# Kernel tuning notes

Hardware: AMD Instinct MI355X
Metric: run time of the kernel (lower is better)

Reference implementation:

```python
import jax, jax.numpy as jnp
import numpy as np

B, L, D, K, H = 2, 384, 1024, 128, 32
NUM_EDGES = 25600
NUM_T = 1000
SCALING = K ** -0.5
SQRT_2PI = float(np.sqrt(2.0 * np.pi))


def setup_inputs() -> dict:
    key = jax.random.key(0)
    ks = jax.random.split(key, 20)
    s = 0.02
    inp = {}
    inp["token_id"] = jax.random.randint(ks[0], (B, L), 0, 160)
    inp["is_periodic"] = jnp.zeros((B,), dtype=bool)
    inp["pos"] = 5.0 * jax.random.normal(ks[1], (B, L, 3), dtype=jnp.float32)
    inp["adj"] = jnp.ones((B, L, L), dtype=bool)
    inp["node_type_edge"] = jax.random.randint(ks[2], (B, L, L, 2), 0, NUM_EDGES)
    inp["time_step"] = jax.random.uniform(ks[3], (B, L), dtype=jnp.float32)
    inp["clean_mask"] = jnp.zeros((B, L), dtype=bool)
    # parameters
    inp["embed_w"] = s * jax.random.normal(ks[4], (160, D), dtype=jnp.float32)
    inp["Wpos"] = s * jax.random.normal(ks[5], (K, 3), dtype=jnp.float32)
    inp["Wpfe"] = s * jax.random.normal(ks[6], (D, K), dtype=jnp.float32)
    inp["gbf_means"] = jax.random.normal(ks[7], (K,), dtype=jnp.float32)
    inp["gbf_stds"] = 0.5 + jax.random.uniform(ks[8], (K,), dtype=jnp.float32)
    inp["gbf_mul"] = 1.0 + s * jax.random.normal(ks[9], (NUM_EDGES, 1), dtype=jnp.float32)
    inp["gbf_bias"] = s * jax.random.normal(ks[10], (NUM_EDGES, 1), dtype=jnp.float32)
    inp["W1"] = s * jax.random.normal(ks[11], (K, K), dtype=jnp.float32)
    inp["b1"] = jnp.zeros((K,), dtype=jnp.float32)
    inp["W2"] = s * jax.random.normal(ks[12], (H, K), dtype=jnp.float32)
    inp["b2"] = jnp.zeros((H,), dtype=jnp.float32)
    inp["Wproj"] = s * jax.random.normal(ks[13], (D, K), dtype=jnp.float32)
    inp["bproj"] = jnp.zeros((D,), dtype=jnp.float32)
    inp["Wt1"] = s * jax.random.normal(ks[14], (D, D), dtype=jnp.float32)
    inp["bt1"] = jnp.zeros((D,), dtype=jnp.float32)
    inp["Wt2"] = s * jax.random.normal(ks[15], (D, D), dtype=jnp.float32)
    inp["bt2"] = jnp.zeros((D,), dtype=jnp.float32)
    return inp


def _forward(token_id, is_periodic, pos, adj, node_type_edge, time_step, clean_mask,
             embed_w, Wpos, Wpfe, gbf_means, gbf_stds, gbf_mul, gbf_bias,
             W1, b1, W2, b2, Wproj, bproj, Wt1, bt1, Wt2, bt2):
    padding_mask = token_id == 0                                  # (B,L)
    molecule_mask = (token_id <= 129) & (~is_periodic[:, None])   # (B,L)
    x = embed_w[token_id]                                         # (B,L,D)

    # ---- _pos_emb (non-PBC branch: expand_pos = pos, expand_mask = padding_mask) ----
    delta = pos[:, :, None, :] - pos[:, None, :, :]               # (B,L,L,3)
    dist = jnp.sqrt(jnp.maximum(jnp.sum(delta * delta, -1), 1e-12))  # (B,L,L), safe norm

    # GaussianLayer
    mul = gbf_mul[node_type_edge].sum(-2)                         # (B,L,L,1)
    bias = gbf_bias[node_type_edge].sum(-2)                       # (B,L,L,1)
    y = mul * dist[..., None] + bias                              # (B,L,L,1) -> broadcast K
    std = jnp.abs(gbf_stds) + 1e-5
    a = (y - gbf_means) / std
    edge_feature = jnp.exp(-0.5 * a * a) / (SQRT_2PI * std)       # (B,L,L,K)

    # NonLinear projection to per-head bias
    gab = jax.nn.gelu(edge_feature @ W1.T + b1, approximate=False) @ W2.T + b2  # (B,L,L,H)
    gab = jnp.where(padding_mask[:, None, :, None], -jnp.inf, gab)  # expand-col mask
    gab = jnp.where(padding_mask[:, :, None, None], 0.0, gab)       # padding-row mask
    pos_attn_bias = jnp.transpose(gab, (0, 3, 1, 2))              # (B,H,L,L)

    d = gab.sum(-1)                                               # (B,L,L) sum over heads
    minv = jnp.finfo(jnp.float32).min
    d = jnp.where(padding_mask[:, None, :], minv, d)
    d = jnp.where(padding_mask[:, :, None], minv, d)
    adj_eff = adj | (~molecule_mask[:, :, None])
    d = jnp.where(~adj_eff, minv, d)
    attn = jax.nn.softmax(d * SCALING, axis=-1)                   # (B,L,L)

    pos_e = pos @ Wpos.T                                          # (B,L,K)
    pos_e = jnp.where(padding_mask[..., None], 0.0, pos_e)
    pfe = jnp.einsum('bij,bjk->bik', attn, pos_e)                 # (B,L,K)
    pfe = pfe @ Wpfe.T                                            # (B,L,D)

    ef = jnp.where(padding_mask[:, None, :, None], 0.0, edge_feature).sum(-2)  # (B,L,K)
    pfe = pfe + ef @ Wproj.T + bproj
    pos_embedding = jnp.where(padding_mask[..., None], 0.0, pfe)  # (B,L,D)

    # ---- time step encoder (sinusoidal + MLP) ----
    t = jnp.where(clean_mask, 0.0, time_step) * NUM_T             # (B,L)
    half = D // 2
    freqs = jnp.exp(-jnp.log(10000.0) * jnp.arange(half, dtype=jnp.float32) / half)
    ang = t[..., None] * freqs                                    # (B,L,half)
    sin_emb = jnp.concatenate([jnp.sin(ang), jnp.cos(ang)], -1)   # (B,L,D)
    time_embed = jax.nn.silu(sin_emb @ Wt1.T + bt1) @ Wt2.T + bt2

    x = x + time_embed + pos_embedding
    return x, padding_mask, time_embed, pos_attn_bias, pos_embedding


def reference(token_id, is_periodic, pos, adj, node_type_edge, time_step, clean_mask,
              embed_w, Wpos, Wpfe, gbf_means, gbf_stds, gbf_mul, gbf_bias,
              W1, b1, W2, b2, Wproj, bproj, Wt1, bt1, Wt2, bt2):
    return _forward(token_id, is_periodic, pos, adj, node_type_edge, time_step, clean_mask,
                    embed_w, Wpos, Wpfe, gbf_means, gbf_stds, gbf_mul, gbf_bias,
                    W1, b1, W2, b2, Wproj, bproj, Wt1, bt1, Wt2, bt2)
```

## Files before the change

kernel.cpp:

```cpp
#include <hip/hip_runtime.h>
#include <stddef.h>

#define B_ 2
#define L_ 384
#define D_ 1024
#define K_ 128
#define H_ 32

#define MINV (-3.402823466e38f)
#define NEG_BIG (-1.0e38f)
#define SCALING_ 0.08838834764831845f
#define INV_SQRT_2PI 0.3989422804014327f

typedef __attribute__((ext_vector_type(8))) short bf16x8;
typedef __attribute__((ext_vector_type(4))) float f32x4;

__device__ __forceinline__ float finitize(float x) {
    return fminf(fmaxf(x, -1.0e38f), 1.0e38f);
}
__device__ __forceinline__ unsigned short f2bf(float x) {
    unsigned int u = __float_as_uint(x);
    u += 0x7FFFu + ((u >> 16) & 1u);
    return (unsigned short)(u >> 16);
}
__device__ __forceinline__ unsigned short f2bf_rtz(float x) {
    return (unsigned short)(__float_as_uint(x) >> 16);
}
__device__ __forceinline__ float gelu_tanh(float x) {
    const float x2 = x * x;
    const float z = x * fmaf(0.0356774081f, x2, 0.7978845608f);
    const float e = __expf(2.0f * z);
    const float t = fmaf(-2.0f, __builtin_amdgcn_rcpf(e + 1.0f), 1.0f);
    const float hx = 0.5f * x;
    return fmaf(hx, t, hx);
}

__global__ __launch_bounds__(256) void prep_kernel(
    const float* __restrict__ W1, const float* __restrict__ W2,
    const float* __restrict__ Wpfe, const float* __restrict__ Wproj,
    const float* __restrict__ Wt1, const float* __restrict__ Wt2,
    unsigned short* __restrict__ W1bf, unsigned short* __restrict__ W2bf,
    unsigned short* __restrict__ Wpfebf, unsigned short* __restrict__ Wprojbf,
    unsigned short* __restrict__ Wt1bf, unsigned short* __restrict__ Wt2bf)
{
    const int i = blockIdx.x * 256 + threadIdx.x;
    const float* src; unsigned short* dst; int off;
    if (i < 4096)        { src = W1;    dst = W1bf;    off = i; }
    else if (i < 5120)   { src = W2;    dst = W2bf;    off = i - 4096; }
    else if (i < 37888)  { src = Wpfe;  dst = Wpfebf;  off = i - 5120; }
    else if (i < 70656)  { src = Wproj; dst = Wprojbf; off = i - 37888; }
    else if (i < 332800) { src = Wt1;   dst = Wt1bf;   off = i - 70656; }
    else if (i < 594944) { src = Wt2;   dst = Wt2bf;   off = i - 332800; }
    else return;
    const float4 v = ((const float4*)src)[off];
    ushort4 p; p.x = f2bf(v.x); p.y = f2bf(v.y); p.z = f2bf(v.z); p.w = f2bf(v.w);
    ((ushort4*)dst)[off] = p;
}

__global__ __launch_bounds__(256) void sin_kernel(const float* __restrict__ time_step,
                                                  const unsigned char* __restrict__ clean,
                                                  const int* __restrict__ token,
                                                  unsigned short* __restrict__ sin_bf,
                                                  float* __restrict__ padout)
{
    const int row = blockIdx.x;
    if (threadIdx.x == 0) padout[row] = (token[row] == 0) ? 1.0f : 0.0f;
    const float t = (clean[row] ? 0.0f : time_step[row]) * 1000.0f;
    for (int k = threadIdx.x; k < 512; k += 256) {
        const float f = __expf(-9.210340371976184f * (float)k * (1.0f / 512.0f));
        const float ang = t * f;
        sin_bf[(size_t)row * D_ + k]       = f2bf(__sinf(ang));
        sin_bf[(size_t)row * D_ + 512 + k] = f2bf(__cosf(ang));
    }
}

__global__ __launch_bounds__(256) void gemm_ts(const unsigned short* __restrict__ A,
                                               const unsigned short* __restrict__ Bw,
                                               const float* __restrict__ bias,
                                               void* __restrict__ Cv,
                                               int M, int N, int Kd, int act)
{
    __shared__ unsigned short sA[32][72];
    __shared__ unsigned short sB[64][72];
    const int tid  = threadIdx.x;
    const int lane = tid & 63;
    const int wave = tid >> 6;
    const int l15  = lane & 15;
    const int quad = lane >> 4;
    const int mt   = wave & 1;
    const int np   = wave >> 1;
    const int m0 = blockIdx.y * 32, n0 = blockIdx.x * 64;

    const int ar = tid >> 3,        ac = (tid & 7) * 8;
    const int br0 = tid >> 3,       bc0 = ac;
    const int br1 = (tid + 256) >> 3, bc1 = ac;

    f32x4 acc[2];
#pragma unroll
    for (int t = 0; t < 2; ++t) acc[t] = (f32x4){0.f, 0.f, 0.f, 0.f};

    uint4 ra  = *(const uint4*)&A[(size_t)(m0 + ar) * Kd + ac];
    uint4 rb0 = *(const uint4*)&Bw[(size_t)(n0 + br0) * Kd + bc0];
    uint4 rb1 = *(const uint4*)&Bw[(size_t)(n0 + br1) * Kd + bc1];

    for (int k0 = 0; k0 < Kd; k0 += 64) {
        *(uint4*)&sA[ar][ac]   = ra;
        *(uint4*)&sB[br0][bc0] = rb0;
        *(uint4*)&sB[br1][bc1] = rb1;
        __syncthreads();
        if (k0 + 64 < Kd) {
            ra  = *(const uint4*)&A[(size_t)(m0 + ar) * Kd + k0 + 64 + ac];
            rb0 = *(const uint4*)&Bw[(size_t)(n0 + br0) * Kd + k0 + 64 + bc0];
            rb1 = *(const uint4*)&Bw[(size_t)(n0 + br1) * Kd + k0 + 64 + bc1];
        }
#pragma unroll
        for (int kk = 0; kk < 64; kk += 32) {
            const bf16x8 av = *(const bf16x8*)&sA[mt * 16 + l15][kk + quad * 8];
#pragma unroll
            for (int t = 0; t < 2; ++t) {
                const bf16x8 bv = *(const bf16x8*)&sB[(np * 2 + t) * 16 + l15][kk + quad * 8];
                acc[t] = __builtin_amdgcn_mfma_f32_16x16x32_bf16(av, bv, acc[t], 0, 0, 0);
            }
        }
        __syncthreads();
    }
#pragma unroll
    for (int t = 0; t < 2; ++t) {
        const int nc = n0 + (np * 2 + t) * 16 + l15;
        const float bv = bias[nc];
#pragma unroll
        for (int r = 0; r < 4; ++r) {
            const int mr = m0 + mt * 16 + quad * 4 + r;
            float v = acc[t][r] + bv;
            if (act) {
                v = v / (1.0f + __expf(-v));
                ((unsigned short*)Cv)[(size_t)mr * N + nc] = f2bf(v);
            } else {
                ((float*)Cv)[(size_t)mr * N + nc] = v;
            }
        }
    }
}

__global__ __launch_bounds__(256) void pe_gemm(const unsigned short* __restrict__ pfe_bf,
                                               const unsigned short* __restrict__ ef_bf,
                                               const unsigned short* __restrict__ Wpfebf,
                                               const unsigned short* __restrict__ Wprojbf,
                                               const float* __restrict__ bproj,
                                               const int* __restrict__ token,
                                               const float* __restrict__ embed_w,
                                               const float* __restrict__ te,
                                               float* __restrict__ outPE,
                                               float* __restrict__ outX)
{
    __shared__ unsigned short sA[32][136];
    __shared__ unsigned short sB[64][136];
    const int tid  = threadIdx.x;
    const int lane = tid & 63;
    const int wave = tid >> 6;
    const int l15  = lane & 15;
    const int quad = lane >> 4;
    const int mt   = wave & 1;
    const int np   = wave >> 1;
    const int m0 = blockIdx.y * 32, n0 = blockIdx.x * 64;

    f32x4 acc[2];
#pragma unroll
    for (int t = 0; t < 2; ++t) acc[t] = (f32x4){0.f, 0.f, 0.f, 0.f};

    for (int phase = 0; phase < 2; ++phase) {
        const unsigned short* Ap = phase ? ef_bf : pfe_bf;
        const unsigned short* Bp = phase ? Wprojbf : Wpfebf;
#pragma unroll
        for (int e = tid; e < 512; e += 256) {
            const int r = e >> 4, c8 = (e & 15) * 8;
            *(uint4*)&sA[r][c8] = *(const uint4*)&Ap[(size_t)(m0 + r) * K_ + c8];
        }
#pragma unroll
        for (int e = tid; e < 1024; e += 256) {
            const int r = e >> 4, c8 = (e & 15) * 8;
            *(uint4*)&sB[r][c8] = *(const uint4*)&Bp[(size_t)(n0 + r) * K_ + c8];
        }
        __syncthreads();
#pragma unroll
        for (int ks = 0; ks < 4; ++ks) {
            const bf16x8 av = *(const bf16x8*)&sA[mt * 16 + l15][ks * 32 + quad * 8];
#pragma unroll
            for (int t = 0; t < 2; ++t) {
                const bf16x8 bv = *(const bf16x8*)&sB[(np * 2 + t) * 16 + l15][ks * 32 + quad * 8];
                acc[t] = __builtin_amdgcn_mfma_f32_16x16x32_bf16(av, bv, acc[t], 0, 0, 0);
            }
        }
        __syncthreads();
    }
#pragma unroll
    for (int t = 0; t < 2; ++t) {
        const int nc = n0 + (np * 2 + t) * 16 + l15;
        const float bv = bproj[nc];
#pragma unroll
        for (int r = 0; r < 4; ++r) {
            const int mr = m0 + mt * 16 + quad * 4 + r;
            const int tok = token[mr];
            const float pe = (tok == 0) ? 0.0f : (acc[t][r] + bv);
            outPE[(size_t)mr * D_ + nc] = pe;
            outX[(size_t)mr * D_ + nc] = embed_w[(size_t)tok * D_ + nc]
                                       + te[(size_t)mr * D_ + nc] + pe;
        }
    }
}

__global__ __launch_bounds__(256, 3) void edge_kernel(
    const int* __restrict__ token_id,
    const unsigned char* __restrict__ is_periodic,
    const float* __restrict__ pos,
    const unsigned char* __restrict__ adj,
    const int* __restrict__ nte,
    const float* __restrict__ gbf_means,
    const float* __restrict__ gbf_stds,
    const float* __restrict__ gbf_mul,
    const float* __restrict__ gbf_bias,
    const float* __restrict__ b1,
    const float* __restrict__ b2,
    const float* __restrict__ Wpos,
    const unsigned short* __restrict__ W1bf,
    const unsigned short* __restrict__ W2bf,
    unsigned short* __restrict__ pfe_bf,
    unsigned short* __restrict__ ef_bf,
    float* __restrict__ out_pab)
{
    const int bx = blockIdx.x;
    const int b = bx / L_;
    const int i = bx - b * L_;
    const int row = bx;
    const int tid = threadIdx.x;

    const int tok_i = token_id[row];
    if (tok_i == 0) {
        for (int idx = tid; idx < H_ * L_; idx += 256) {
            const int h = idx / L_;
            const int j = idx - h * L_;
            out_pab[((size_t)(b * H_ + h) * L_ + i) * L_ + j] = 0.0f;
        }
        if (tid < K_) {
            pfe_bf[(size_t)row * K_ + tid] = 0;
            ef_bf[(size_t)row * K_ + tid]  = 0;
        }
        return;
    }

    __shared__ unsigned short sEF[2][32][136];
    __shared__ unsigned short sACT[32][136];
    __shared__ float sGab[32][33];
    __shared__ float sD[L_];
    __shared__ float sRed[256];
    __shared__ float sYall[L_];
    __shared__ unsigned char sPadCol[L_];

    for (int j = tid; j < L_; j += 256)
        sPadCol[j] = (token_id[b * L_ + j] == 0) ? 1 : 0;

    const float px = pos[(size_t)row * 3 + 0];
    const float py = pos[(size_t)row * 3 + 1];
    const float pz = pos[(size_t)row * 3 + 2];
    for (int jg2 = tid; jg2 < L_; jg2 += 256) {
        const float dx = px - pos[(size_t)(b * L_ + jg2) * 3 + 0];
        const float dy = py - pos[(size_t)(b * L_ + jg2) * 3 + 1];
        const float dz = pz - pos[(size_t)(b * L_ + jg2) * 3 + 2];
        const float dist = sqrtf(fmaxf(dx * dx + dy * dy + dz * dz, 1e-12f));
        const size_t eoff = ((size_t)(b * L_ + i) * L_ + jg2) * 2;
        const int e0 = nte[eoff], e1 = nte[eoff + 1];
        sYall[jg2] = (gbf_mul[e0] + gbf_mul[e1]) * dist + (gbf_bias[e0] + gbf_bias[e1]);
    }

    const int lane = tid & 63;
    const int wave = tid >> 6;
    const int l15  = lane & 15;
    const int quad = lane >> 4;
    const int mt   = wave & 1;
    const int ntb  = (wave >> 1) * 4;
    float rb1[4];
#pragma unroll
    for (int nt = 0; nt < 4; ++nt) rb1[nt] = b1[(ntb + nt) * 16 + l15];
    const int hc = (wave >> 1) * 16 + l15;
    const float rb2 = b2[hc];
    bf16x8 w1f[4][4];
#pragma unroll
    for (int ks = 0; ks < 4; ++ks)
#pragma unroll
        for (int nt = 0; nt < 4; ++nt)
            w1f[ks][nt] = *(const bf16x8*)&W1bf[((ntb + nt) * 16 + l15) * K_ + ks * 32 + quad * 8];
    bf16x8 bv2[4];
#pragma unroll
    for (int ks = 0; ks < 4; ++ks)
        bv2[ks] = *(const bf16x8*)&W2bf[hc * K_ + ks * 32 + quad * 8];

    const int kg4 = (tid & 31) * 4;
    const int jg  = tid >> 5;
    const int jb  = jg * 4;
    float meanv[4], istdv[4], cKv[4];
#pragma unroll
    for (int c = 0; c < 4; ++c) {
        meanv[c] = gbf_means[kg4 + c];
        const float s = fabsf(gbf_stds[kg4 + c]) + 1e-5f;
        istdv[c] = 1.0f / s;
        cKv[c]   = INV_SQRT_2PI * istdv[c];
    }
    float efs[4] = {0.f, 0.f, 0.f, 0.f};

    __syncthreads();

#pragma unroll
    for (int jj = 0; jj < 4; ++jj) {
        const int j = jb + jj;
        const float y = sYall[j];
        const bool ok = !sPadCol[j];
        ushort4 p;
#pragma unroll
        for (int c = 0; c < 4; ++c) {
            const float a = (y - meanv[c]) * istdv[c];
            const float ef = __expf(-0.5f * a * a) * cKv[c];
            ((unsigned short*)&p)[c] = f2bf_rtz(ef);
            if (ok) efs[c] += ef;
        }
        *(ushort4*)&sEF[0][j][kg4] = p;
    }
    __syncthreads();

    for (int tile = 0; tile < L_ / 32; ++tile) {
        const int jt0 = tile * 32;
        const int cur = tile & 1, nxt = cur ^ 1;

        f32x4 acc1[4];
#pragma unroll
        for (int nt = 0; nt < 4; ++nt) acc1[nt] = (f32x4){0.f, 0.f, 0.f, 0.f};
#pragma unroll
        for (int ks = 0; ks < 4; ++ks) {
            const bf16x8 av = *(const bf16x8*)&sEF[cur][mt * 16 + l15][ks * 32 + quad * 8];
#pragma unroll
            for (int nt = 0; nt < 4; ++nt)
                acc1[nt] = __builtin_amdgcn_mfma_f32_16x16x32_bf16(av, w1f[ks][nt], acc1[nt], 0, 0, 0);
        }

        if (tile + 1 < L_ / 32) {
            const int jn0 = jt0 + 32;
#pragma unroll
            for (int jj = 0; jj < 4; ++jj) {
                const int j = jb + jj;
                const float y = sYall[jn0 + j];
                const bool ok = !sPadCol[jn0 + j];
                ushort4 p;
#pragma unroll
                for (int c = 0; c < 4; ++c) {
                    const float a = (y - meanv[c]) * istdv[c];
                    const float ef = __expf(-0.5f * a * a) * cKv[c];
                    ((unsigned short*)&p)[c] = f2bf_rtz(ef);
                    if (ok) efs[c] += ef;
                }
                *(ushort4*)&sEF[nxt][j][kg4] = p;
            }
        }

#pragma unroll
        for (int nt = 0; nt < 4; ++nt) {
            const int kkc = (ntb + nt) * 16 + l15;
#pragma unroll
            for (int r = 0; r < 4; ++r) {
                const float v = gelu_tanh(acc1[nt][r] + rb1[nt]);
                sACT[mt * 16 + quad * 4 + r][kkc] = f2bf_rtz(v);
            }
        }
        __syncthreads();

        f32x4 acc2 = (f32x4){0.f, 0.f, 0.f, 0.f};
#pragma unroll
        for (int ks = 0; ks < 4; ++ks) {
            const bf16x8 av = *(const bf16x8*)&sACT[mt * 16 + l15][ks * 32 + quad * 8];
            acc2 = __builtin_amdgcn_mfma_f32_16x16x32_bf16(av, bv2[ks], acc2, 0, 0, 0);
        }
        const int jl0 = mt * 16 + quad * 4;
#pragma unroll
        for (int r = 0; r < 4; ++r) sGab[jl0 + r][hc] = acc2[r] + rb2;
        __syncthreads();

        {
            const int h = tid >> 3, f = tid & 7;
            const int jb2 = f * 4;
            float4 st;
#pragma unroll
            for (int r = 0; r < 4; ++r) {
                float v = finitize(sGab[jb2 + r][h]);
                if (sPadCol[jt0 + jb2 + r]) v = NEG_BIG;
                ((float*)&st)[r] = v;
            }
            *(float4*)&out_pab[((size_t)(b * H_ + h) * L_ + i) * L_ + jt0 + jb2] = st;
        }
        if (tid < 32) {
            float s = 0.0f;
#pragma unroll
            for (int h = 0; h < 32; ++h) s += sGab[tid][h];
            sD[jt0 + tid] = s;
        }
    }

    {
        float* efScr = (float*)sACT;
#pragma unroll
        for (int c = 0; c < 4; ++c) efScr[jg * 128 + kg4 + c] = efs[c];
    }
    __syncthreads();
    if (tid < 128) {
        const float* efScr = (const float*)sACT;
        float s = 0.0f;
#pragma unroll
        for (int g = 0; g < 8; ++g) s += efScr[g * 128 + tid];
        ef_bf[(size_t)row * K_ + tid] = f2bf(s);
    }
    __syncthreads();

    const int lane2 = tid & 63;
    const int wave2 = tid >> 6;
    const bool molecule = (tok_i <= 129) && (is_periodic[b] == 0);
    float lmax = -INFINITY;
    for (int j = tid; j < L_; j += 256) {
        const bool colpad = sPadCol[j] != 0;
        const bool adj_eff = (adj[((size_t)(b * L_ + i)) * L_ + j] != 0) || (!molecule);
        const float dv = (colpad || !adj_eff) ? MINV : sD[j];
        const float s = dv * SCALING_;
        sD[j] = s;
        lmax = fmaxf(lmax, s);
    }
#pragma unroll
    for (int off = 32; off > 0; off >>= 1) lmax = fmaxf(lmax, __shfl_xor(lmax, off));
    if (lane2 == 0) sRed[wave2] = lmax;
    __syncthreads();
    const float smax = fmaxf(fmaxf(sRed[0], sRed[1]), fmaxf(sRed[2], sRed[3]));
    float lsum = 0.0f;
    for (int j = tid; j < L_; j += 256) {
        const float e = __expf(sD[j] - smax);
        sD[j] = e;
        lsum += e;
    }
#pragma unroll
    for (int off = 32; off > 0; off >>= 1) lsum += __shfl_xor(lsum, off);
    if (lane2 == 0) sRed[4 + wave2] = lsum;
    __syncthreads();
    const float inv = 1.0f / (sRed[4] + sRed[5] + sRed[6] + sRed[7]);

    float a0 = 0.f, a1 = 0.f, a2 = 0.f;
    for (int j = tid; j < L_; j += 256) {
        if (!sPadCol[j]) {
            const float e = sD[j];
            a0 += e * pos[(size_t)(b * L_ + j) * 3 + 0];
            a1 += e * pos[(size_t)(b * L_ + j) * 3 + 1];
            a2 += e * pos[(size_t)(b * L_ + j) * 3 + 2];
        }
    }
#pragma unroll
    for (int off = 32; off > 0; off >>= 1) {
        a0 += __shfl_xor(a0, off);
        a1 += __shfl_xor(a1, off);
        a2 += __shfl_xor(a2, off);
    }
    if (lane2 == 0) { sRed[8 + wave2] = a0; sRed[12 + wave2] = a1; sRed[16 + wave2] = a2; }
    __syncthreads();
    if (tid < 128) {
        const float m0 = sRed[8] + sRed[9] + sRed[10] + sRed[11];
        const float m1 = sRed[12] + sRed[13] + sRed[14] + sRed[15];
        const float m2 = sRed[16] + sRed[17] + sRed[18] + sRed[19];
        const float w0 = Wpos[tid * 3 + 0], w1 = Wpos[tid * 3 + 1], w2 = Wpos[tid * 3 + 2];
        pfe_bf[(size_t)row * K_ + tid] = f2bf((m0 * w0 + m1 * w1 + m2 * w2) * inv);
    }
}

extern "C" void kernel_launch(void* const* d_in, const int* in_sizes, int n_in,
                              void* d_out, int out_size, void* d_ws, size_t ws_size,
                              hipStream_t stream) {
    const int*           token_id    = (const int*)d_in[0];
    const unsigned char* is_periodic = (const unsigned char*)d_in[1];
    const float*         pos         = (const float*)d_in[2];
    const unsigned char* adj         = (const unsigned char*)d_in[3];
    const int*           nte         = (const int*)d_in[4];
    const float*         time_step   = (const float*)d_in[5];
    const unsigned char* clean_mask  = (const unsigned char*)d_in[6];
    const float*         embed_w     = (const float*)d_in[7];
    const float*         Wpos        = (const float*)d_in[8];
    const float*         Wpfe        = (const float*)d_in[9];
    const float*         gbf_means   = (const float*)d_in[10];
    const float*         gbf_stds    = (const float*)d_in[11];
    const float*         gbf_mul     = (const float*)d_in[12];
    const float*         gbf_bias    = (const float*)d_in[13];
    const float*         W1          = (const float*)d_in[14];
    const float*         b1          = (const float*)d_in[15];
    const float*         W2          = (const float*)d_in[16];
    const float*         b2          = (const float*)d_in[17];
    const float*         Wproj       = (const float*)d_in[18];
    const float*         bproj       = (const float*)d_in[19];
    const float*         Wt1         = (const float*)d_in[20];
    const float*         bt1         = (const float*)d_in[21];
    const float*         Wt2         = (const float*)d_in[22];
    const float*         bt2         = (const float*)d_in[23];

    float* out = (float*)d_out;
    float* out_x   = out;
    float* out_pad = out + 786432;
    float* out_te  = out + 787200;
    float* out_pab = out + 1573632;
    float* out_pe  = out + 11010816;

    unsigned short* wsu = (unsigned short*)d_ws;
    unsigned short* W1bf    = wsu;
    unsigned short* W2bf    = wsu + 16384;
    unsigned short* Wpfebf  = wsu + 20480;
    unsigned short* Wprojbf = wsu + 151552;
    unsigned short* sin_bf  = wsu + 282624;
    unsigned short* h1_bf   = wsu + 1069056;
    unsigned short* pfe_bf  = wsu + 1855488;
    unsigned short* ef_bf   = wsu + 1953792;
    unsigned short* Wt1bf = (unsigned short*)out_pab;
    unsigned short* Wt2bf = Wt1bf + 1048576;

    prep_kernel<<<dim3(2325), dim3(256), 0, stream>>>(W1, W2, Wpfe, Wproj, Wt1, Wt2,
                                                      W1bf, W2bf, Wpfebf, Wprojbf,
                                                      Wt1bf, Wt2bf);
    sin_kernel<<<dim3(B_ * L_), dim3(256), 0, stream>>>(time_step, clean_mask, token_id,
                                                        sin_bf, out_pad);
    gemm_ts<<<dim3(16, 24), dim3(256), 0, stream>>>(sin_bf, Wt1bf, bt1, (void*)h1_bf,
                                                    768, 1024, 1024, 1);
    gemm_ts<<<dim3(16, 24), dim3(256), 0, stream>>>(h1_bf, Wt2bf, bt2, (void*)out_te,
                                                    768, 1024, 1024, 0);
    edge_kernel<<<dim3(B_ * L_), dim3(256), 0, stream>>>(
        token_id, is_periodic, pos, adj, nte, gbf_means, gbf_stds, gbf_mul, gbf_bias,
        b1, b2, Wpos, W1bf, W2bf, pfe_bf, ef_bf, out_pab);
    pe_gemm<<<dim3(16, 24), dim3(256), 0, stream>>>(pfe_bf, ef_bf, Wpfebf, Wprojbf,
                                                    bproj, token_id, embed_w, out_te,
                                                    out_pe, out_x);
}
```

Measured before the change: 194.6 us.

## Split edge kernel across column halves, merge prep and sin kernels, widen GEMM K-tile

The edge kernel now runs two blocks per row, each covering half of the columns, and writes partial distance sums and edge-feature partials to scratch held in the pos-embedding output buffer. A new post kernel then does the softmax, the position weighting and the merge of the edge-feature partials. The weight-prep and sinusoid kernels are fused into one launch, and the time GEMM K-tile grows from 64 to 128 so it syncs less often. The aim is more parallelism in the edge stage (768 to 1536 blocks, higher occupancy) and fewer launches, at the cost of an extra launch and a round trip through global scratch.

```diff
diff --git a/kernel.cpp b/kernel.cpp
--- a/kernel.cpp
+++ b/kernel.cpp
@@ -35,42 +35,40 @@
     return fmaf(hx, t, hx);
 }
 
-__global__ __launch_bounds__(256) void prep_kernel(
+__global__ __launch_bounds__(256) void prep_sin_kernel(
     const float* __restrict__ W1, const float* __restrict__ W2,
     const float* __restrict__ Wpfe, const float* __restrict__ Wproj,
     const float* __restrict__ Wt1, const float* __restrict__ Wt2,
     unsigned short* __restrict__ W1bf, unsigned short* __restrict__ W2bf,
     unsigned short* __restrict__ Wpfebf, unsigned short* __restrict__ Wprojbf,
-    unsigned short* __restrict__ Wt1bf, unsigned short* __restrict__ Wt2bf)
+    unsigned short* __restrict__ Wt1bf, unsigned short* __restrict__ Wt2bf,
+    const float* __restrict__ time_step, const unsigned char* __restrict__ clean,
+    const int* __restrict__ token, unsigned short* __restrict__ sin_bf,
+    float* __restrict__ padout)
 {
-    const int i = blockIdx.x * 256 + threadIdx.x;
-    const float* src; unsigned short* dst; int off;
-    if (i < 4096)        { src = W1;    dst = W1bf;    off = i; }
-    else if (i < 5120)   { src = W2;    dst = W2bf;    off = i - 4096; }
-    else if (i < 37888)  { src = Wpfe;  dst = Wpfebf;  off = i - 5120; }
-    else if (i < 70656)  { src = Wproj; dst = Wprojbf; off = i - 37888; }
-    else if (i < 332800) { src = Wt1;   dst = Wt1bf;   off = i - 70656; }
-    else if (i < 594944) { src = Wt2;   dst = Wt2bf;   off = i - 332800; }
-    else return;
-    const float4 v = ((const float4*)src)[off];
-    ushort4 p; p.x = f2bf(v.x); p.y = f2bf(v.y); p.z = f2bf(v.z); p.w = f2bf(v.w);
-    ((ushort4*)dst)[off] = p;
-}
-
-__global__ __launch_bounds__(256) void sin_kernel(const float* __restrict__ time_step,
-                                                  const unsigned char* __restrict__ clean,
-                                                  const int* __restrict__ token,
-                                                  unsigned short* __restrict__ sin_bf,
-                                                  float* __restrict__ padout)
-{
-    const int row = blockIdx.x;
-    if (threadIdx.x == 0) padout[row] = (token[row] == 0) ? 1.0f : 0.0f;
-    const float t = (clean[row] ? 0.0f : time_step[row]) * 1000.0f;
-    for (int k = threadIdx.x; k < 512; k += 256) {
-        const float f = __expf(-9.210340371976184f * (float)k * (1.0f / 512.0f));
-        const float ang = t * f;
-        sin_bf[(size_t)row * D_ + k]       = f2bf(__sinf(ang));
-        sin_bf[(size_t)row * D_ + 512 + k] = f2bf(__cosf(ang));
+    const int blk = blockIdx.x;
+    if (blk < 2324) {
+        const int i = blk * 256 + threadIdx.x;
+        const float* src; unsigned short* dst; int off;
+        if (i < 4096)        { src = W1;    dst = W1bf;    off = i; }
+        else if (i < 5120)   { src = W2;    dst = W2bf;    off = i - 4096; }
+        else if (i < 37888)  { src = Wpfe;  dst = Wpfebf;  off = i - 5120; }
+        else if (i < 70656)  { src = Wproj; dst = Wprojbf; off = i - 37888; }
+        else if (i < 332800) { src = Wt1;   dst = Wt1bf;   off = i - 70656; }
+        else                 { src = Wt2;   dst = Wt2bf;   off = i - 332800; }
+        const float4 v = ((const float4*)src)[off];
+        ushort4 p; p.x = f2bf(v.x); p.y = f2bf(v.y); p.z = f2bf(v.z); p.w = f2bf(v.w);
+        ((ushort4*)dst)[off] = p;
+    } else {
+        const int row = blk - 2324;
+        if (threadIdx.x == 0) padout[row] = (token[row] == 0) ? 1.0f : 0.0f;
+        const float t = (clean[row] ? 0.0f : time_step[row]) * 1000.0f;
+        for (int k = threadIdx.x; k < 512; k += 256) {
+            const float f = __expf(-9.210340371976184f * (float)k * (1.0f / 512.0f));
+            const float ang = t * f;
+            sin_bf[(size_t)row * D_ + k]       = f2bf(__sinf(ang));
+            sin_bf[(size_t)row * D_ + 512 + k] = f2bf(__cosf(ang));
+        }
     }
 }
 
@@ -80,8 +78,8 @@
                                                void* __restrict__ Cv,
                                                int M, int N, int Kd, int act)
 {
-    __shared__ unsigned short sA[32][72];
-    __shared__ unsigned short sB[64][72];
+    __shared__ unsigned short sA[32][136];
+    __shared__ unsigned short sB[64][136];
     const int tid  = threadIdx.x;
     const int lane = tid & 63;
     const int wave = tid >> 6;
@@ -91,30 +89,35 @@
     const int np   = wave >> 1;
     const int m0 = blockIdx.y * 32, n0 = blockIdx.x * 64;
 
-    const int ar = tid >> 3,        ac = (tid & 7) * 8;
-    const int br0 = tid >> 3,       bc0 = ac;
-    const int br1 = (tid + 256) >> 3, bc1 = ac;
+    const int c8  = (tid & 15) * 8;
+    const int ar0 = tid >> 4, ar1 = (tid + 256) >> 4;
 
     f32x4 acc[2];
 #pragma unroll
     for (int t = 0; t < 2; ++t) acc[t] = (f32x4){0.f, 0.f, 0.f, 0.f};
 
-    uint4 ra  = *(const uint4*)&A[(size_t)(m0 + ar) * Kd + ac];
-    uint4 rb0 = *(const uint4*)&Bw[(size_t)(n0 + br0) * Kd + bc0];
-    uint4 rb1 = *(const uint4*)&Bw[(size_t)(n0 + br1) * Kd + bc1];
-
-    for (int k0 = 0; k0 < Kd; k0 += 64) {
-        *(uint4*)&sA[ar][ac]   = ra;
-        *(uint4*)&sB[br0][bc0] = rb0;
-        *(uint4*)&sB[br1][bc1] = rb1;
+    uint4 ra0 = *(const uint4*)&A[(size_t)(m0 + ar0) * Kd + c8];
+    uint4 ra1 = *(const uint4*)&A[(size_t)(m0 + ar1) * Kd + c8];
+    uint4 rb[4];
+#pragma unroll
+    for (int c = 0; c < 4; ++c)
+        rb[c] = *(const uint4*)&Bw[(size_t)(n0 + ((tid + c * 256) >> 4)) * Kd + c8];
+
+    for (int k0 = 0; k0 < Kd; k0 += 128) {
+        *(uint4*)&sA[ar0][c8] = ra0;
+        *(uint4*)&sA[ar1][c8] = ra1;
+#pragma unroll
+        for (int c = 0; c < 4; ++c) *(uint4*)&sB[(tid + c * 256) >> 4][c8] = rb[c];
         __syncthreads();
-        if (k0 + 64 < Kd) {
-            ra  = *(const uint4*)&A[(size_t)(m0 + ar) * Kd + k0 + 64 + ac];
-            rb0 = *(const uint4*)&Bw[(size_t)(n0 + br0) * Kd + k0 + 64 + bc0];
-            rb1 = *(const uint4*)&Bw[(size_t)(n0 + br1) * Kd + k0 + 64 + bc1];
-        }
-#pragma unroll
-        for (int kk = 0; kk < 64; kk += 32) {
+        if (k0 + 128 < Kd) {
+            ra0 = *(const uint4*)&A[(size_t)(m0 + ar0) * Kd + k0 + 128 + c8];
+            ra1 = *(const uint4*)&A[(size_t)(m0 + ar1) * Kd + k0 + 128 + c8];
+#pragma unroll
+            for (int c = 0; c < 4; ++c)
+                rb[c] = *(const uint4*)&Bw[(size_t)(n0 + ((tid + c * 256) >> 4)) * Kd + k0 + 128 + c8];
+        }
+#pragma unroll
+        for (int kk = 0; kk < 128; kk += 32) {
             const bf16x8 av = *(const bf16x8*)&sA[mt * 16 + l15][kk + quad * 8];
 #pragma unroll
             for (int t = 0; t < 2; ++t) {
@@ -209,11 +212,9 @@
     }
 }
 
-__global__ __launch_bounds__(256, 3) void edge_kernel(
+__global__ __launch_bounds__(256, 4) void edge_main(
     const int* __restrict__ token_id,
-    const unsigned char* __restrict__ is_periodic,
     const float* __restrict__ pos,
-    const unsigned char* __restrict__ adj,
     const int* __restrict__ nte,
     const float* __restrict__ gbf_means,
     const float* __restrict__ gbf_stds,
@@ -221,29 +222,25 @@
     const float* __restrict__ gbf_bias,
     const float* __restrict__ b1,
     const float* __restrict__ b2,
-    const float* __restrict__ Wpos,
     const unsigned short* __restrict__ W1bf,
     const unsigned short* __restrict__ W2bf,
-    unsigned short* __restrict__ pfe_bf,
-    unsigned short* __restrict__ ef_bf,
+    float* __restrict__ ws_d,
+    float* __restrict__ ws_efp,
     float* __restrict__ out_pab)
 {
     const int bx = blockIdx.x;
-    const int b = bx / L_;
-    const int i = bx - b * L_;
-    const int row = bx;
+    const int row = bx >> 1;
+    const int half = bx & 1;
+    const int b = row / L_;
+    const int i = row - b * L_;
+    const int j0 = half * 192;
     const int tid = threadIdx.x;
 
     const int tok_i = token_id[row];
     if (tok_i == 0) {
-        for (int idx = tid; idx < H_ * L_; idx += 256) {
-            const int h = idx / L_;
-            const int j = idx - h * L_;
-            out_pab[((size_t)(b * H_ + h) * L_ + i) * L_ + j] = 0.0f;
-        }
-        if (tid < K_) {
-            pfe_bf[(size_t)row * K_ + tid] = 0;
-            ef_bf[(size_t)row * K_ + tid]  = 0;
+        for (int idx = tid; idx < H_ * 192; idx += 256) {
+            const int h = idx / 192, j = idx - h * 192;
+            out_pab[((size_t)(b * H_ + h) * L_ + i) * L_ + j0 + j] = 0.0f;
         }
         return;
     }
@@ -251,25 +248,24 @@
     __shared__ unsigned short sEF[2][32][136];
     __shared__ unsigned short sACT[32][136];
     __shared__ float sGab[32][33];
-    __shared__ float sD[L_];
-    __shared__ float sRed[256];
-    __shared__ float sYall[L_];
-    __shared__ unsigned char sPadCol[L_];
-
-    for (int j = tid; j < L_; j += 256)
-        sPadCol[j] = (token_id[b * L_ + j] == 0) ? 1 : 0;
+    __shared__ float sY[192];
+    __shared__ unsigned char sPadCol[192];
+
+    for (int jl = tid; jl < 192; jl += 256)
+        sPadCol[jl] = (token_id[b * L_ + j0 + jl] == 0) ? 1 : 0;
 
     const float px = pos[(size_t)row * 3 + 0];
     const float py = pos[(size_t)row * 3 + 1];
     const float pz = pos[(size_t)row * 3 + 2];
-    for (int jg2 = tid; jg2 < L_; jg2 += 256) {
+    for (int jl = tid; jl < 192; jl += 256) {
+        const int jg2 = j0 + jl;
         const float dx = px - pos[(size_t)(b * L_ + jg2) * 3 + 0];
         const float dy = py - pos[(size_t)(b * L_ + jg2) * 3 + 1];
         const float dz = pz - pos[(size_t)(b * L_ + jg2) * 3 + 2];
         const float dist = sqrtf(fmaxf(dx * dx + dy * dy + dz * dz, 1e-12f));
         const size_t eoff = ((size_t)(b * L_ + i) * L_ + jg2) * 2;
         const int e0 = nte[eoff], e1 = nte[eoff + 1];
-        sYall[jg2] = (gbf_mul[e0] + gbf_mul[e1]) * dist + (gbf_bias[e0] + gbf_bias[e1]);
+        sY[jl] = (gbf_mul[e0] + gbf_mul[e1]) * dist + (gbf_bias[e0] + gbf_bias[e1]);
     }
 
     const int lane = tid & 63;
@@ -312,7 +308,7 @@
 #pragma unroll
     for (int jj = 0; jj < 4; ++jj) {
         const int j = jb + jj;
-        const float y = sYall[j];
+        const float y = sY[j];
         const bool ok = !sPadCol[j];
         ushort4 p;
 #pragma unroll
@@ -326,7 +322,7 @@
     }
     __syncthreads();
 
-    for (int tile = 0; tile < L_ / 32; ++tile) {
+    for (int tile = 0; tile < 6; ++tile) {
         const int jt0 = tile * 32;
         const int cur = tile & 1, nxt = cur ^ 1;
 
@@ -341,12 +337,12 @@
                 acc1[nt] = __builtin_amdgcn_mfma_f32_16x16x32_bf16(av, w1f[ks][nt], acc1[nt], 0, 0, 0);
         }
 
-        if (tile + 1 < L_ / 32) {
+        if (tile + 1 < 6) {
             const int jn0 = jt0 + 32;
 #pragma unroll
             for (int jj = 0; jj < 4; ++jj) {
                 const int j = jb + jj;
-                const float y = sYall[jn0 + j];
+                const float y = sY[jn0 + j];
                 const bool ok = !sPadCol[jn0 + j];
                 ushort4 p;
 #pragma unroll
@@ -392,13 +388,13 @@
                 if (sPadCol[jt0 + jb2 + r]) v = NEG_BIG;
                 ((float*)&st)[r] = v;
             }
-            *(float4*)&out_pab[((size_t)(b * H_ + h) * L_ + i) * L_ + jt0 + jb2] = st;
+            *(float4*)&out_pab[((size_t)(b * H_ + h) * L_ + i) * L_ + j0 + jt0 + jb2] = st;
         }
         if (tid < 32) {
             float s = 0.0f;
 #pragma unroll
             for (int h = 0; h < 32; ++h) s += sGab[tid][h];
-            sD[jt0 + tid] = s;
+            ws_d[(size_t)row * L_ + j0 + jt0 + tid] = s;
         }
     }
 
@@ -413,25 +409,54 @@
         float s = 0.0f;
 #pragma unroll
         for (int g = 0; g < 8; ++g) s += efScr[g * 128 + tid];
-        ef_bf[(size_t)row * K_ + tid] = f2bf(s);
-    }
-    __syncthreads();
-
-    const int lane2 = tid & 63;
-    const int wave2 = tid >> 6;
-    const bool molecule = (tok_i <= 129) && (is_periodic[b] == 0);
+        ws_efp[((size_t)row * 2 + half) * 128 + tid] = s;
+    }
+}
+
+__global__ __launch_bounds__(256) void edge_post(
+    const int* __restrict__ token_id,
+    const unsigned char* __restrict__ is_periodic,
+    const float* __restrict__ pos,
+    const unsigned char* __restrict__ adj,
+    const float* __restrict__ Wpos,
+    const float* __restrict__ ws_d,
+    const float* __restrict__ ws_efp,
+    unsigned short* __restrict__ pfe_bf,
+    unsigned short* __restrict__ ef_bf)
+{
+    const int row = blockIdx.x;
+    const int tid = threadIdx.x;
+    const int tok = token_id[row];
+    if (tok == 0) {
+        if (tid < 128) {
+            pfe_bf[(size_t)row * K_ + tid] = 0;
+            ef_bf[(size_t)row * K_ + tid]  = 0;
+        }
+        return;
+    }
+    const int b = row / L_;
+    const int i = row - b * L_;
+    const int lane = tid & 63;
+    const int wave = tid >> 6;
+
+    __shared__ float sD[L_];
+    __shared__ unsigned char sPad[L_];
+    __shared__ float sRed[32];
+
+    const bool molecule = (tok <= 129) && (is_periodic[b] == 0);
     float lmax = -INFINITY;
     for (int j = tid; j < L_; j += 256) {
-        const bool colpad = sPadCol[j] != 0;
-        const bool adj_eff = (adj[((size_t)(b * L_ + i)) * L_ + j] != 0) || (!molecule);
-        const float dv = (colpad || !adj_eff) ? MINV : sD[j];
+        const bool colpad = (token_id[b * L_ + j] == 0);
+        sPad[j] = colpad ? 1 : 0;
+        const bool ae = (adj[(size_t)(b * L_ + i) * L_ + j] != 0) || (!molecule);
+        const float dv = (colpad || !ae) ? MINV : ws_d[(size_t)row * L_ + j];
         const float s = dv * SCALING_;
         sD[j] = s;
         lmax = fmaxf(lmax, s);
     }
 #pragma unroll
     for (int off = 32; off > 0; off >>= 1) lmax = fmaxf(lmax, __shfl_xor(lmax, off));
-    if (lane2 == 0) sRed[wave2] = lmax;
+    if (lane == 0) sRed[wave] = lmax;
     __syncthreads();
     const float smax = fmaxf(fmaxf(sRed[0], sRed[1]), fmaxf(sRed[2], sRed[3]));
     float lsum = 0.0f;
@@ -442,13 +467,13 @@
     }
 #pragma unroll
     for (int off = 32; off > 0; off >>= 1) lsum += __shfl_xor(lsum, off);
-    if (lane2 == 0) sRed[4 + wave2] = lsum;
+    if (lane == 0) sRed[4 + wave] = lsum;
     __syncthreads();
     const float inv = 1.0f / (sRed[4] + sRed[5] + sRed[6] + sRed[7]);
 
     float a0 = 0.f, a1 = 0.f, a2 = 0.f;
     for (int j = tid; j < L_; j += 256) {
-        if (!sPadCol[j]) {
+        if (!sPad[j]) {
             const float e = sD[j];
             a0 += e * pos[(size_t)(b * L_ + j) * 3 + 0];
             a1 += e * pos[(size_t)(b * L_ + j) * 3 + 1];
@@ -461,7 +486,7 @@
         a1 += __shfl_xor(a1, off);
         a2 += __shfl_xor(a2, off);
     }
-    if (lane2 == 0) { sRed[8 + wave2] = a0; sRed[12 + wave2] = a1; sRed[16 + wave2] = a2; }
+    if (lane == 0) { sRed[8 + wave] = a0; sRed[12 + wave] = a1; sRed[16 + wave] = a2; }
     __syncthreads();
     if (tid < 128) {
         const float m0 = sRed[8] + sRed[9] + sRed[10] + sRed[11];
@@ -469,6 +494,8 @@
         const float m2 = sRed[16] + sRed[17] + sRed[18] + sRed[19];
         const float w0 = Wpos[tid * 3 + 0], w1 = Wpos[tid * 3 + 1], w2 = Wpos[tid * 3 + 2];
         pfe_bf[(size_t)row * K_ + tid] = f2bf((m0 * w0 + m1 * w1 + m2 * w2) * inv);
+        ef_bf[(size_t)row * K_ + tid] =
+            f2bf(ws_efp[(size_t)row * 256 + tid] + ws_efp[(size_t)row * 256 + 128 + tid]);
     }
 }
 
@@ -518,19 +545,22 @@
     unsigned short* ef_bf   = wsu + 1953792;
     unsigned short* Wt1bf = (unsigned short*)out_pab;
     unsigned short* Wt2bf = Wt1bf + 1048576;
-
-    prep_kernel<<<dim3(2325), dim3(256), 0, stream>>>(W1, W2, Wpfe, Wproj, Wt1, Wt2,
-                                                      W1bf, W2bf, Wpfebf, Wprojbf,
-                                                      Wt1bf, Wt2bf);
-    sin_kernel<<<dim3(B_ * L_), dim3(256), 0, stream>>>(time_step, clean_mask, token_id,
-                                                        sin_bf, out_pad);
+    float* ws_d   = out_pe;
+    float* ws_efp = out_pe + 294912;
+
+    prep_sin_kernel<<<dim3(3092), dim3(256), 0, stream>>>(
+        W1, W2, Wpfe, Wproj, Wt1, Wt2,
+        W1bf, W2bf, Wpfebf, Wprojbf, Wt1bf, Wt2bf,
+        time_step, clean_mask, token_id, sin_bf, out_pad);
     gemm_ts<<<dim3(16, 24), dim3(256), 0, stream>>>(sin_bf, Wt1bf, bt1, (void*)h1_bf,
                                                     768, 1024, 1024, 1);
     gemm_ts<<<dim3(16, 24), dim3(256), 0, stream>>>(h1_bf, Wt2bf, bt2, (void*)out_te,
                                                     768, 1024, 1024, 0);
-    edge_kernel<<<dim3(B_ * L_), dim3(256), 0, stream>>>(
-        token_id, is_periodic, pos, adj, nte, gbf_means, gbf_stds, gbf_mul, gbf_bias,
-        b1, b2, Wpos, W1bf, W2bf, pfe_bf, ef_bf, out_pab);
+    edge_main<<<dim3(2 * B_ * L_), dim3(256), 0, stream>>>(
+        token_id, pos, nte, gbf_means, gbf_stds, gbf_mul, gbf_bias,
+        b1, b2, W1bf, W2bf, ws_d, ws_efp, out_pab);
+    edge_post<<<dim3(B_ * L_), dim3(256), 0, stream>>>(
+        token_id, is_periodic, pos, adj, Wpos, ws_d, ws_efp, pfe_bf, ef_bf);
     pe_gemm<<<dim3(16, 24), dim3(256), 0, stream>>>(pfe_bf, ef_bf, Wpfebf, Wprojbf,
                                                     bproj, token_id, embed_w, out_te,
                                                     out_pe, out_x);
```

Result: slower. 264.5 us (+35.9%).
